# Kernel tuning notes

Hardware: AMD Instinct MI355X
Metric: run time of the kernel (lower is better)

Reference implementation:

```python
import jax, jax.numpy as jnp
import numpy as np

IN_DIM = 256
OUT_DIM = 64   # per-head dim
NUM_HEADS = 8
B = 8
N = 1024


def setup_inputs() -> dict:
    key = jax.random.key(0)
    k_adj, k_h, kq, kk, kv, kbq, kbk, kbv = jax.random.split(key, 8)
    adj_matrix = jax.random.randint(k_adj, (N, N), 0, 2, dtype=jnp.int32)
    h = jax.random.normal(k_h, (B, N, IN_DIM), dtype=jnp.float32)
    s = 1.0 / np.sqrt(IN_DIM)
    Wq = jax.random.normal(kq, (IN_DIM, OUT_DIM * NUM_HEADS), dtype=jnp.float32) * s
    Wk = jax.random.normal(kk, (IN_DIM, OUT_DIM * NUM_HEADS), dtype=jnp.float32) * s
    Wv = jax.random.normal(kv, (IN_DIM, OUT_DIM * NUM_HEADS), dtype=jnp.float32) * s
    bq = jax.random.normal(kbq, (OUT_DIM * NUM_HEADS,), dtype=jnp.float32) * 0.01
    bk = jax.random.normal(kbk, (OUT_DIM * NUM_HEADS,), dtype=jnp.float32) * 0.01
    bv = jax.random.normal(kbv, (OUT_DIM * NUM_HEADS,), dtype=jnp.float32) * 0.01
    return {"adj_matrix": adj_matrix, "h": h, "Wq": Wq, "bq": bq,
            "Wk": Wk, "bk": bk, "Wv": Wv, "bv": bv}


def reference(adj_matrix, h, Wq, bq, Wk, bk, Wv, bv):
    B_, N_, _ = h.shape
    H, D = NUM_HEADS, OUT_DIM
    Qh = (h @ Wq + bq).reshape(B_, N_, H, D)
    Kh = (h @ Wk + bk).reshape(B_, N_, H, D)
    Vh = (h @ Wv + bv).reshape(B_, N_, H, D)
    scores = jnp.einsum('bnhd,bmhd->bhnm', Qh, Kh) / jnp.sqrt(jnp.float32(D))
    # adjacency mask broadcast over batch and heads (neigh_attention=True)
    scores = jnp.where(adj_matrix[None, None, :, :] == 0, -jnp.inf, scores)
    attn = jax.nn.softmax(scores, axis=-1)
    out = jnp.einsum('bhnm,bmhd->bnhd', attn, Vh)
    return out.reshape(B_, N_, H * D)
```

## Files before the change

### kernel.cpp

```cpp
#include <hip/hip_runtime.h>
#include <hip/hip_bf16.h>
#include <math.h>

#define IN_DIM 256
#define HD     512
#define NHEADS 8
#define DH     64
#define NSEQ   1024
#define BATCH  8

#define QSCALE 0.18033688011112042f

typedef unsigned short u16;
typedef unsigned int   u32;
typedef short bf16x8 __attribute__((ext_vector_type(8)));
typedef float f32x4  __attribute__((ext_vector_type(4)));
typedef float f32x16 __attribute__((ext_vector_type(16)));
typedef unsigned int u32x2 __attribute__((ext_vector_type(2)));

#if __has_builtin(__builtin_amdgcn_exp2f)
#define EXP2(x) __builtin_amdgcn_exp2f(x)
#else
#define EXP2(x) __expf(0.69314718056f * (x))
#endif

static __device__ __forceinline__ u16 f2bf(float x) {
    u32 u = __builtin_bit_cast(u32, x);
    u += 0x7FFFu + ((u >> 16) & 1u);
    return (u16)(u >> 16);
}
static __device__ __forceinline__ u32 pk(u16 a, u16 b) {
    return (u32)a | ((u32)b << 16);
}
static __device__ __forceinline__ u32 cvtpk(float a, float b) {
    __hip_bfloat162 t = __float22bfloat162_rn(make_float2(a, b));
    u32 r; __builtin_memcpy(&r, &t, 4);
    return r;
}
static __device__ __forceinline__ f32x16 maskinit(uint4 a, uint4 b) {
    f32x16 c;
    u32 ws[8] = {a.x, a.y, a.z, a.w, b.x, b.y, b.z, b.w};
#pragma unroll
    for (int i = 0; i < 8; ++i) {
        c[2 * i]     = __builtin_bit_cast(float, ws[i] << 16);
        c[2 * i + 1] = __builtin_bit_cast(float, ws[i] & 0xFFFF0000u);
    }
    return c;
}

static __device__ __forceinline__ void pswap(u32 &a, u32 &b) {
#if __has_builtin(__builtin_amdgcn_permlane32_swap)
    u32x2 r = __builtin_amdgcn_permlane32_swap(a, b, false, false);
    a = r.x; b = r.y;
#else
    const bool hi = (threadIdx.x & 32) != 0;
    u32 as = (u32)__shfl_xor((int)a, 32, 64);
    u32 bs = (u32)__shfl_xor((int)b, 32, 64);
    u32 na = hi ? bs : a;
    u32 nb = hi ? b  : as;
    a = na; b = nb;
#endif
}

#define MFMA32(a, b, c) __builtin_amdgcn_mfma_f32_32x32x16_bf16(a, b, c, 0, 0, 0)

static __device__ __forceinline__ float sm_pack(const f32x16 s0, const f32x16 s1,
                                                bf16x8* pb) {
    float p0[16], p1[16];
#pragma unroll
    for (int r = 0; r < 16; ++r) p0[r] = EXP2(s0[r]);
#pragma unroll
    for (int r = 0; r < 16; ++r) p1[r] = EXP2(s1[r]);
    float t0 = (((p0[0] + p0[1]) + (p0[2] + p0[3])) + ((p0[4] + p0[5]) + (p0[6] + p0[7])))
             + (((p0[8] + p0[9]) + (p0[10] + p0[11])) + ((p0[12] + p0[13]) + (p0[14] + p0[15])));
    float t1 = (((p1[0] + p1[1]) + (p1[2] + p1[3])) + ((p1[4] + p1[5]) + (p1[6] + p1[7])))
             + (((p1[8] + p1[9]) + (p1[10] + p1[11])) + ((p1[12] + p1[13]) + (p1[14] + p1[15])));
    uint4 w0, w1, w2, w3;
    w0.x = cvtpk(p0[0], p0[1]);   w0.y = cvtpk(p0[2], p0[3]);
    w0.z = cvtpk(p0[4], p0[5]);   w0.w = cvtpk(p0[6], p0[7]);
    w1.x = cvtpk(p0[8], p0[9]);   w1.y = cvtpk(p0[10], p0[11]);
    w1.z = cvtpk(p0[12], p0[13]); w1.w = cvtpk(p0[14], p0[15]);
    w2.x = cvtpk(p1[0], p1[1]);   w2.y = cvtpk(p1[2], p1[3]);
    w2.z = cvtpk(p1[4], p1[5]);   w2.w = cvtpk(p1[6], p1[7]);
    w3.x = cvtpk(p1[8], p1[9]);   w3.y = cvtpk(p1[10], p1[11]);
    w3.z = cvtpk(p1[12], p1[13]); w3.w = cvtpk(p1[14], p1[15]);
    pswap(w0.x, w1.x); pswap(w0.y, w1.y); pswap(w0.z, w1.z); pswap(w0.w, w1.w);
    pswap(w2.x, w3.x); pswap(w2.y, w3.y); pswap(w2.z, w3.z); pswap(w2.w, w3.w);
    pb[0] = __builtin_bit_cast(bf16x8, w0);
    pb[1] = __builtin_bit_cast(bf16x8, w1);
    pb[2] = __builtin_bit_cast(bf16x8, w2);
    pb[3] = __builtin_bit_cast(bf16x8, w3);
    return t0 + t1;
}

__global__ __launch_bounds__(256)
void wtrans_kernel(const float* __restrict__ Wq, const float* __restrict__ Wk,
                   const float* __restrict__ Wv, u16* __restrict__ Wt)
{
    __shared__ float tile[64 * 65];
    const int bid = blockIdx.x, tid = threadIdx.x;
    const int k0 = (bid & 3) * 64, n0 = ((bid >> 2) & 7) * 64, wsel = bid >> 5;
    const float* W = (wsel == 0) ? Wq : (wsel == 1) ? Wk : Wv;
    u16* Out = Wt + (size_t)wsel * HD * IN_DIM;

    const int r = tid >> 2, c0 = (tid & 3) * 16;
#pragma unroll
    for (int j = 0; j < 16; j += 4) {
        float4 v = *(const float4*)(W + (size_t)(k0 + r) * HD + n0 + c0 + j);
        tile[r * 65 + c0 + j + 0] = v.x; tile[r * 65 + c0 + j + 1] = v.y;
        tile[r * 65 + c0 + j + 2] = v.z; tile[r * 65 + c0 + j + 3] = v.w;
    }
    __syncthreads();
    const int n = tid >> 2, ks = (tid & 3) * 16;
    u16 o[16];
#pragma unroll
    for (int j = 0; j < 16; ++j) o[j] = f2bf(tile[(ks + j) * 65 + n]);
    uint4 u0, u1;
    u0.x = pk(o[0], o[1]);   u0.y = pk(o[2], o[3]);
    u0.z = pk(o[4], o[5]);   u0.w = pk(o[6], o[7]);
    u1.x = pk(o[8], o[9]);   u1.y = pk(o[10], o[11]);
    u1.z = pk(o[12], o[13]); u1.w = pk(o[14], o[15]);
    u16* dst = Out + (size_t)(n0 + n) * IN_DIM + k0 + ks;
    *(uint4*)(dst) = u0;
    *(uint4*)(dst + 8) = u1;
}

__global__ __launch_bounds__(256, 4)
void gemm_mask_kernel(const float* __restrict__ h, const u16* __restrict__ Wt,
                      const int* __restrict__ adj,
                      const float* __restrict__ bq, const float* __restrict__ bk,
                      const float* __restrict__ bv,
                      u16* __restrict__ Qg, u16* __restrict__ Kg,
                      u16* __restrict__ Vtg, u16* __restrict__ Madd2)
{
    __shared__ u16 pool[64 * 64 + 3 * 64 * 64];
    const int tid = threadIdx.x;

    if (blockIdx.y >= 8) {
        int* tile = (int*)pool;
        const int abid = (blockIdx.y - 8) * 128 + blockIdx.x;
        const int tR = abid >> 4, tC = abid & 15;
        const int r = tid >> 2, cg = (tid & 3) * 16;
        const int* src = adj + (size_t)(tR * 64 + r) * NSEQ + tC * 64 + cg;
#pragma unroll
        for (int j = 0; j < 16; j += 4) {
            int4 a = *(const int4*)(src + j);
            tile[r * 65 + cg + j + 0] = a.x; tile[r * 65 + cg + j + 1] = a.y;
            tile[r * 65 + cg + j + 2] = a.z; tile[r * 65 + cg + j + 3] = a.w;
        }
        __syncthreads();
        const int q = tid >> 2, p0 = (tid & 3) * 16;
        u16 o[16];
#pragma unroll
        for (int j = 0; j < 16; ++j) {
            const int p = p0 + j;
            const int c = 32 * (p >> 5) + (p & 3) + 4 * ((p >> 4) & 1) + 8 * ((p >> 2) & 3);
            o[j] = (tile[q * 65 + c] == 0) ? (u16)0xFF7F : (u16)0;
        }
        uint4 u0, u1;
        u0.x = pk(o[0], o[1]);   u0.y = pk(o[2], o[3]);
        u0.z = pk(o[4], o[5]);   u0.w = pk(o[6], o[7]);
        u1.x = pk(o[8], o[9]);   u1.y = pk(o[10], o[11]);
        u1.z = pk(o[12], o[13]); u1.w = pk(o[14], o[15]);
        u16* dst = Madd2 + (size_t)(tR * 64 + q) * NSEQ + tC * 64 + p0;
        *(uint4*)(dst) = u0;
        *(uint4*)(dst + 8) = u1;
        return;
    }

    u16* As = pool;
    u16* Bs = pool + 64 * 64;

    const int m0 = blockIdx.x * 64;
    const int hh = blockIdx.y;
    const int n0 = hh * 64;

    const int w = tid >> 6, lane = tid & 63;
    const int l31 = lane & 31, half = lane >> 5;
    const int mh = w & 1, nh = w >> 1;
    const int s7 = l31 & 7;

    f32x16 acc[3] = {};

    const int arw = tid >> 2, acg = (tid & 3) * 2;
    const int brw = tid & 63, bgrp = tid >> 6;
    const float* srcA = h + (size_t)(m0 + arw) * IN_DIM;

    for (int kk = 0; kk < IN_DIM; kk += 64) {
        __syncthreads();
#pragma unroll
        for (int g = 0; g < 2; ++g) {
            const float* p = srcA + kk + (acg + g) * 8;
            float4 v0 = *(const float4*)(p);
            float4 v1 = *(const float4*)(p + 4);
            uint4 u;
            u.x = cvtpk(v0.x, v0.y); u.y = cvtpk(v0.z, v0.w);
            u.z = cvtpk(v1.x, v1.y); u.w = cvtpk(v1.z, v1.w);
            *(uint4*)&As[arw * 64 + (((acg + g) ^ (arw & 7)) * 8)] = u;
        }
#pragma unroll
        for (int i = 0; i < 6; ++i) {
            const int gc = bgrp * 6 + i;
            const int wh = gc >> 3, c8 = gc & 7;
            *(uint4*)&Bs[wh * 4096 + brw * 64 + ((c8 ^ (brw & 7)) * 8)] =
                *(const uint4*)(Wt + (size_t)wh * HD * IN_DIM +
                                (size_t)(n0 + brw) * IN_DIM + kk + c8 * 8);
        }
        __syncthreads();
        const int arow = (32 * mh + l31) * 64;
        const int brow = (32 * nh + l31) * 64;
#pragma unroll
        for (int s = 0; s < 4; ++s) {
            const int g = ((s * 2 + half) ^ s7) * 8;
            bf16x8 a = *(const bf16x8*)&As[arow + g];
#pragma unroll
            for (int wh = 0; wh < 3; ++wh) {
                bf16x8 b = *(const bf16x8*)&Bs[wh * 4096 + brow + g];
                acc[wh] = __builtin_amdgcn_mfma_f32_32x32x16_bf16(a, b, acc[wh], 0, 0, 0);
            }
        }
    }

    for (int which = 0; which < 2; ++which) {
        u16* T = pool;
        const float* bias = (which == 0) ? bq : bk;
        u16* Out = (which == 0) ? Qg : Kg;
        const float scale = (which == 0) ? QSCALE : 1.0f;
        const float bvv = bias[n0 + 32 * nh + l31];
        __syncthreads();
#pragma unroll
        for (int r = 0; r < 16; ++r) {
            const int row = 32 * mh + 4 * half + (r & 3) + 8 * (r >> 2);
            T[row * 72 + 32 * nh + l31] = f2bf((acc[which][r] + bvv) * scale);
        }
        __syncthreads();
        const int row = tid >> 2, qc = (tid & 3) * 16;
        u16* dst = Out + (size_t)(m0 + row) * HD + n0 + qc;
        const u16* srcT = &T[row * 72 + qc];
        *(uint4*)(dst)     = *(const uint4*)(srcT);
        *(uint4*)(dst + 8) = *(const uint4*)(srcT + 8);
    }

    {
        u16* T = pool;
        const int d = 32 * nh + l31;
        const float bvv = bv[n0 + d];
        __syncthreads();
#pragma unroll
        for (int g = 0; g < 4; ++g) {
            ushort4 o;
            o.x = f2bf(acc[2][4 * g + 0] + bvv);
            o.y = f2bf(acc[2][4 * g + 1] + bvv);
            o.z = f2bf(acc[2][4 * g + 2] + bvv);
            o.w = f2bf(acc[2][4 * g + 3] + bvv);
            *(ushort4*)&T[d * 72 + 32 * mh + 16 * half + 4 * g] = o;
        }
        __syncthreads();
        const int b = m0 >> 10, nloc = m0 & 1023;
        const int dd = tid >> 2, c = (tid & 3) * 16;
        u16* dst = Vtg + ((size_t)(b * NHEADS + hh) * DH + dd) * NSEQ + nloc + c;
        *(uint4*)(dst)     = *(uint4*)&T[dd * 72 + c];
        *(uint4*)(dst + 8) = *(uint4*)&T[dd * 72 + c + 8];
    }
}

__global__ __launch_bounds__(256, 1)
void attn_kernel(const u16* __restrict__ Madd2, const u16* __restrict__ Qg,
                 const u16* __restrict__ Kg, const u16* __restrict__ Vtg,
                 float* __restrict__ out)
{
    __shared__ u16 Ks[2][64 * 64];
    __shared__ u16 Vs[2][64 * 64];

    const int tid = threadIdx.x;
    const int w = tid >> 6, lane = tid & 63;
    const int l31 = lane & 31, half = lane >> 5;
    const int bh = blockIdx.x, qt = blockIdx.y;
    const int b = bh >> 3;
    const int n0 = qt * 256;
    const size_t rowbase = (size_t)b * NSEQ;
    const int colbase = (bh & 7) * DH;
    const int q7 = l31 & 7;
    const int qA = w * 64 + l31;
    const int qB = qA + 32;

    const u16* qga = Qg + (rowbase + n0 + qA) * HD + colbase;
    const u16* qgb = Qg + (rowbase + n0 + qB) * HD + colbase;
    bf16x8 qbA[4], qbB[4];
#pragma unroll
    for (int s = 0; s < 4; ++s) {
        qbA[s] = *(const bf16x8*)(qga + s * 16 + half * 8);
        qbB[s] = *(const bf16x8*)(qgb + s * 16 + half * 8);
    }

    const int srow = tid >> 2, cp = (tid & 3) * 2;
    const int swc0 = ((cp ^ (srow & 7)) * 8), swc1 = (((cp + 1) ^ (srow & 7)) * 8);
    const u16* kgp = Kg + (rowbase + srow) * HD + colbase + cp * 8;
    const u16* vgp = Vtg + ((size_t)bh * DH + srow) * NSEQ + cp * 8;
    const u16* mrowA = Madd2 + (size_t)(n0 + qA) * NSEQ + half * 16;
    const u16* mrowB = Madd2 + (size_t)(n0 + qB) * NSEQ + half * 16;

    uint4 mA0a = *(const uint4*)(mrowA);
    uint4 mA0b = *(const uint4*)(mrowA + 8);
    uint4 mA1a = *(const uint4*)(mrowA + 32);
    uint4 mA1b = *(const uint4*)(mrowA + 40);
    uint4 mB0a = *(const uint4*)(mrowB);
    uint4 mB0b = *(const uint4*)(mrowB + 8);
    uint4 mB1a = *(const uint4*)(mrowB + 32);
    uint4 mB1b = *(const uint4*)(mrowB + 40);

    uint4 s0k0, s0k1, s0v0, s0v1;
    uint4 s1k0, s1k1, s1v0, s1v1;
    s0k0 = *(const uint4*)kgp;       s0k1 = *(const uint4*)(kgp + 8);
    s0v0 = *(const uint4*)vgp;       s0v1 = *(const uint4*)(vgp + 8);
    *(uint4*)&Ks[0][srow * 64 + swc0] = s0k0;
    *(uint4*)&Ks[0][srow * 64 + swc1] = s0k1;
    *(uint4*)&Vs[0][srow * 64 + swc0] = s0v0;
    *(uint4*)&Vs[0][srow * 64 + swc1] = s0v1;
    s1k0 = *(const uint4*)(kgp + (size_t)64 * HD);
    s1k1 = *(const uint4*)(kgp + (size_t)64 * HD + 8);
    s1v0 = *(const uint4*)(vgp + 64);
    s1v1 = *(const uint4*)(vgp + 64 + 8);
    __syncthreads();

    float lA = 0.f, lB = 0.f;
    f32x16 OA0 = {}, OA1 = {}, OB0 = {}, OB1 = {};

#define CHUNK(CH, CUR, KW, KL)                                                 \
    {                                                                          \
        f32x16 sA0 = maskinit(mA0a, mA0b);                                     \
        f32x16 sA1 = maskinit(mA1a, mA1b);                                     \
        f32x16 sB0 = maskinit(mB0a, mB0b);                                     \
        f32x16 sB1 = maskinit(mB1a, mB1b);                                     \
        if ((CH) < 15) {                                                       \
            const u16* ma = mrowA + ((CH) + 1) * 64;                           \
            const u16* mb = mrowB + ((CH) + 1) * 64;                           \
            mA0a = *(const uint4*)(ma);      mA0b = *(const uint4*)(ma + 8);   \
            mA1a = *(const uint4*)(ma + 32); mA1b = *(const uint4*)(ma + 40);  \
            mB0a = *(const uint4*)(mb);      mB0b = *(const uint4*)(mb + 8);   \
            mB1a = *(const uint4*)(mb + 32); mB1b = *(const uint4*)(mb + 40);  \
        }                                                                      \
        _Pragma("unroll")                                                      \
        for (int s = 0; s < 4; ++s) {                                          \
            const int g = ((s * 2 + half) ^ q7) * 8;                           \
            bf16x8 ka0 = *(const bf16x8*)&Ks[CUR][l31 * 64 + g];               \
            bf16x8 ka1 = *(const bf16x8*)&Ks[CUR][(32 + l31) * 64 + g];        \
            sA0 = MFMA32(ka0, qbA[s], sA0);                                    \
            sA1 = MFMA32(ka1, qbA[s], sA1);                                    \
            sB0 = MFMA32(ka0, qbB[s], sB0);                                    \
            sB1 = MFMA32(ka1, qbB[s], sB1);                                    \
        }                                                                      \
        if ((CH) < 15) {                                                       \
            *(uint4*)&Ks[1 - (CUR)][srow * 64 + swc0] = KW##k0;                \
            *(uint4*)&Ks[1 - (CUR)][srow * 64 + swc1] = KW##k1;                \
            *(uint4*)&Vs[1 - (CUR)][srow * 64 + swc0] = KW##v0;                \
            *(uint4*)&Vs[1 - (CUR)][srow * 64 + swc1] = KW##v1;                \
        }                                                                      \
        if ((CH) < 14) {                                                       \
            const size_t ko = (size_t)((CH) + 2) * 64 * HD;                    \
            const int    vo = ((CH) + 2) * 64;                                 \
            KL##k0 = *(const uint4*)(kgp + ko);                                \
            KL##k1 = *(const uint4*)(kgp + ko + 8);                            \
            KL##v0 = *(const uint4*)(vgp + vo);                                \
            KL##v1 = *(const uint4*)(vgp + vo + 8);                            \
        }                                                                      \
        bf16x8 pbA[4], pbB[4];                                                 \
        lA += sm_pack(sA0, sA1, pbA);                                          \
        lB += sm_pack(sB0, sB1, pbB);                                          \
        _Pragma("unroll")                                                      \
        for (int s = 0; s < 4; ++s) {                                          \
            const int g = ((s * 2 + half) ^ q7) * 8;                           \
            bf16x8 va0 = *(const bf16x8*)&Vs[CUR][l31 * 64 + g];               \
            bf16x8 va1 = *(const bf16x8*)&Vs[CUR][(32 + l31) * 64 + g];        \
            OA0 = MFMA32(va0, pbA[s], OA0);                                    \
            OA1 = MFMA32(va1, pbA[s], OA1);                                    \
            OB0 = MFMA32(va0, pbB[s], OB0);                                    \
            OB1 = MFMA32(va1, pbB[s], OB1);                                    \
        }                                                                      \
        __syncthreads();                                                       \
    }

    for (int ch = 0; ch < 16; ch += 2) {
        CHUNK(ch,     0, s1, s0)
        CHUNK(ch + 1, 1, s0, s1)
    }
#undef CHUNK

    lA += __shfl_xor(lA, 32, 64);
    lB += __shfl_xor(lB, 32, 64);
    const float invA = 1.0f / lA;
    const float invB = 1.0f / lB;

    float* orowA = out + (rowbase + n0 + qA) * HD + colbase;
    float* orowB = out + (rowbase + n0 + qB) * HD + colbase;
#pragma unroll
    for (int g = 0; g < 4; ++g) {
        const int d0 = 4 * half + 8 * g;
        float4 a0, a1, b0, b1;
        a0.x = OA0[4 * g + 0] * invA; a0.y = OA0[4 * g + 1] * invA;
        a0.z = OA0[4 * g + 2] * invA; a0.w = OA0[4 * g + 3] * invA;
        a1.x = OA1[4 * g + 0] * invA; a1.y = OA1[4 * g + 1] * invA;
        a1.z = OA1[4 * g + 2] * invA; a1.w = OA1[4 * g + 3] * invA;
        b0.x = OB0[4 * g + 0] * invB; b0.y = OB0[4 * g + 1] * invB;
        b0.z = OB0[4 * g + 2] * invB; b0.w = OB0[4 * g + 3] * invB;
        b1.x = OB1[4 * g + 0] * invB; b1.y = OB1[4 * g + 1] * invB;
        b1.z = OB1[4 * g + 2] * invB; b1.w = OB1[4 * g + 3] * invB;
        *(float4*)(orowA + d0)      = a0;
        *(float4*)(orowA + 32 + d0) = a1;
        *(float4*)(orowB + d0)      = b0;
        *(float4*)(orowB + 32 + d0) = b1;
    }
}

extern "C" void kernel_launch(void* const* d_in, const int* in_sizes, int n_in,
                              void* d_out, int out_size, void* d_ws, size_t ws_size,
                              hipStream_t stream) {
    const int*   adj = (const int*)d_in[0];
    const float* h   = (const float*)d_in[1];
    const float* Wq  = (const float*)d_in[2];
    const float* bq  = (const float*)d_in[3];
    const float* Wk  = (const float*)d_in[4];
    const float* bk  = (const float*)d_in[5];
    const float* Wv  = (const float*)d_in[6];
    const float* bv  = (const float*)d_in[7];
    float* outp = (float*)d_out;

    u16* Wt    = (u16*)d_ws;
    u16* Qg    = Wt + (size_t)3 * HD * IN_DIM;
    u16* Kg    = Qg + (size_t)BATCH * NSEQ * HD;
    u16* Vtg   = Kg + (size_t)BATCH * NSEQ * HD;
    u16* Madd2 = Vtg + (size_t)BATCH * NSEQ * HD;
    (void)ws_size;

    wtrans_kernel<<<96, 256, 0, stream>>>(Wq, Wk, Wv, Wt);
    gemm_mask_kernel<<<dim3(BATCH * NSEQ / 64, 10), 256, 0, stream>>>(
        h, Wt, adj, bq, bk, bv, Qg, Kg, Vtg, Madd2);
    attn_kernel<<<dim3(BATCH * NHEADS, NSEQ / 256), 256, 0, stream>>>(
        Madd2, Qg, Kg, Vtg, outp);
}
```

Measured before the change: 136.0 us.

## Split attention key range across two wave teams with LDS reduction

The attention block grows to 512 threads in two teams of four waves. Each team processes half of the key/value sequence with its own double-buffered LDS tiles. Partial outputs and row sums are then reduced through LDS before team 0 normalizes and writes. This doubles the waves per block to improve latency hiding and shortens the serial chunk loop, at the cost of extra LDS, a cross-team reduction, and possible register pressure under the new launch bounds. The scheme relies on the softmax having no running-max rescale, so the two halves' partial sums can simply be added.

```diff
diff --git a/kernel.cpp b/kernel.cpp
--- a/kernel.cpp
+++ b/kernel.cpp
@@ -264,16 +264,17 @@
     }
 }
 
-__global__ __launch_bounds__(256, 1)
+__global__ __launch_bounds__(512, 2)
 void attn_kernel(const u16* __restrict__ Madd2, const u16* __restrict__ Qg,
                  const u16* __restrict__ Kg, const u16* __restrict__ Vtg,
                  float* __restrict__ out)
 {
-    __shared__ u16 Ks[2][64 * 64];
-    __shared__ u16 Vs[2][64 * 64];
+    __shared__ __align__(16) u16 Ks[2][2][64 * 64];
+    __shared__ __align__(16) u16 Vs[2][2][64 * 64];
 
     const int tid = threadIdx.x;
     const int w = tid >> 6, lane = tid & 63;
+    const int team = w >> 2, wq = w & 3;
     const int l31 = lane & 31, half = lane >> 5;
     const int bh = blockIdx.x, qt = blockIdx.y;
     const int b = bh >> 3;
@@ -281,8 +282,9 @@
     const size_t rowbase = (size_t)b * NSEQ;
     const int colbase = (bh & 7) * DH;
     const int q7 = l31 & 7;
-    const int qA = w * 64 + l31;
+    const int qA = wq * 64 + l31;
     const int qB = qA + 32;
+    const int cbase = team * 8;
 
     const u16* qga = Qg + (rowbase + n0 + qA) * HD + colbase;
     const u16* qgb = Qg + (rowbase + n0 + qB) * HD + colbase;
@@ -293,12 +295,14 @@
         qbB[s] = *(const bf16x8*)(qgb + s * 16 + half * 8);
     }
 
-    const int srow = tid >> 2, cp = (tid & 3) * 2;
+    const int ttid = tid & 255;
+    const int srow = ttid >> 2, cp = (ttid & 3) * 2;
     const int swc0 = ((cp ^ (srow & 7)) * 8), swc1 = (((cp + 1) ^ (srow & 7)) * 8);
-    const u16* kgp = Kg + (rowbase + srow) * HD + colbase + cp * 8;
-    const u16* vgp = Vtg + ((size_t)bh * DH + srow) * NSEQ + cp * 8;
-    const u16* mrowA = Madd2 + (size_t)(n0 + qA) * NSEQ + half * 16;
-    const u16* mrowB = Madd2 + (size_t)(n0 + qB) * NSEQ + half * 16;
+    const u16* kgp = Kg + (rowbase + srow) * HD + colbase + cp * 8 +
+                     (size_t)cbase * 64 * HD;
+    const u16* vgp = Vtg + ((size_t)bh * DH + srow) * NSEQ + cp * 8 + cbase * 64;
+    const u16* mrowA = Madd2 + (size_t)(n0 + qA) * NSEQ + half * 16 + cbase * 64;
+    const u16* mrowB = Madd2 + (size_t)(n0 + qB) * NSEQ + half * 16 + cbase * 64;
 
     uint4 mA0a = *(const uint4*)(mrowA);
     uint4 mA0b = *(const uint4*)(mrowA + 8);
@@ -313,10 +317,10 @@
     uint4 s1k0, s1k1, s1v0, s1v1;
     s0k0 = *(const uint4*)kgp;       s0k1 = *(const uint4*)(kgp + 8);
     s0v0 = *(const uint4*)vgp;       s0v1 = *(const uint4*)(vgp + 8);
-    *(uint4*)&Ks[0][srow * 64 + swc0] = s0k0;
-    *(uint4*)&Ks[0][srow * 64 + swc1] = s0k1;
-    *(uint4*)&Vs[0][srow * 64 + swc0] = s0v0;
-    *(uint4*)&Vs[0][srow * 64 + swc1] = s0v1;
+    *(uint4*)&Ks[team][0][srow * 64 + swc0] = s0k0;
+    *(uint4*)&Ks[team][0][srow * 64 + swc1] = s0k1;
+    *(uint4*)&Vs[team][0][srow * 64 + swc0] = s0v0;
+    *(uint4*)&Vs[team][0][srow * 64 + swc1] = s0v1;
     s1k0 = *(const uint4*)(kgp + (size_t)64 * HD);
     s1k1 = *(const uint4*)(kgp + (size_t)64 * HD + 8);
     s1v0 = *(const uint4*)(vgp + 64);
@@ -332,7 +336,7 @@
         f32x16 sA1 = maskinit(mA1a, mA1b);                                     \
         f32x16 sB0 = maskinit(mB0a, mB0b);                                     \
         f32x16 sB1 = maskinit(mB1a, mB1b);                                     \
-        if ((CH) < 15) {                                                       \
+        if ((CH) < 7) {                                                        \
             const u16* ma = mrowA + ((CH) + 1) * 64;                           \
             const u16* mb = mrowB + ((CH) + 1) * 64;                           \
             mA0a = *(const uint4*)(ma);      mA0b = *(const uint4*)(ma + 8);   \
@@ -343,20 +347,20 @@
         _Pragma("unroll")                                                      \
         for (int s = 0; s < 4; ++s) {                                          \
             const int g = ((s * 2 + half) ^ q7) * 8;                           \
-            bf16x8 ka0 = *(const bf16x8*)&Ks[CUR][l31 * 64 + g];               \
-            bf16x8 ka1 = *(const bf16x8*)&Ks[CUR][(32 + l31) * 64 + g];        \
+            bf16x8 ka0 = *(const bf16x8*)&Ks[team][CUR][l31 * 64 + g];         \
+            bf16x8 ka1 = *(const bf16x8*)&Ks[team][CUR][(32 + l31) * 64 + g];  \
             sA0 = MFMA32(ka0, qbA[s], sA0);                                    \
             sA1 = MFMA32(ka1, qbA[s], sA1);                                    \
             sB0 = MFMA32(ka0, qbB[s], sB0);                                    \
             sB1 = MFMA32(ka1, qbB[s], sB1);                                    \
         }                                                                      \
-        if ((CH) < 15) {                                                       \
-            *(uint4*)&Ks[1 - (CUR)][srow * 64 + swc0] = KW##k0;                \
-            *(uint4*)&Ks[1 - (CUR)][srow * 64 + swc1] = KW##k1;                \
-            *(uint4*)&Vs[1 - (CUR)][srow * 64 + swc0] = KW##v0;                \
-            *(uint4*)&Vs[1 - (CUR)][srow * 64 + swc1] = KW##v1;                \
+        if ((CH) < 7) {                                                        \
+            *(uint4*)&Ks[team][1 - (CUR)][srow * 64 + swc0] = KW##k0;          \
+            *(uint4*)&Ks[team][1 - (CUR)][srow * 64 + swc1] = KW##k1;          \
+            *(uint4*)&Vs[team][1 - (CUR)][srow * 64 + swc0] = KW##v0;          \
+            *(uint4*)&Vs[team][1 - (CUR)][srow * 64 + swc1] = KW##v1;          \
         }                                                                      \
-        if ((CH) < 14) {                                                       \
+        if ((CH) < 6) {                                                        \
             const size_t ko = (size_t)((CH) + 2) * 64 * HD;                    \
             const int    vo = ((CH) + 2) * 64;                                 \
             KL##k0 = *(const uint4*)(kgp + ko);                                \
@@ -370,8 +374,8 @@
         _Pragma("unroll")                                                      \
         for (int s = 0; s < 4; ++s) {                                          \
             const int g = ((s * 2 + half) ^ q7) * 8;                           \
-            bf16x8 va0 = *(const bf16x8*)&Vs[CUR][l31 * 64 + g];               \
-            bf16x8 va1 = *(const bf16x8*)&Vs[CUR][(32 + l31) * 64 + g];        \
+            bf16x8 va0 = *(const bf16x8*)&Vs[team][CUR][l31 * 64 + g];         \
+            bf16x8 va1 = *(const bf16x8*)&Vs[team][CUR][(32 + l31) * 64 + g];  \
             OA0 = MFMA32(va0, pbA[s], OA0);                                    \
             OA1 = MFMA32(va1, pbA[s], OA1);                                    \
             OB0 = MFMA32(va0, pbB[s], OB0);                                    \
@@ -380,35 +384,92 @@
         __syncthreads();                                                       \
     }
 
-    for (int ch = 0; ch < 16; ch += 2) {
+    for (int ch = 0; ch < 8; ch += 2) {
         CHUNK(ch,     0, s1, s0)
         CHUNK(ch + 1, 1, s0, s1)
     }
 #undef CHUNK
 
-    lA += __shfl_xor(lA, 32, 64);
-    lB += __shfl_xor(lB, 32, 64);
-    const float invA = 1.0f / lA;
-    const float invB = 1.0f / lB;
-
-    float* orowA = out + (rowbase + n0 + qA) * HD + colbase;
-    float* orowB = out + (rowbase + n0 + qB) * HD + colbase;
-#pragma unroll
-    for (int g = 0; g < 4; ++g) {
-        const int d0 = 4 * half + 8 * g;
-        float4 a0, a1, b0, b1;
-        a0.x = OA0[4 * g + 0] * invA; a0.y = OA0[4 * g + 1] * invA;
-        a0.z = OA0[4 * g + 2] * invA; a0.w = OA0[4 * g + 3] * invA;
-        a1.x = OA1[4 * g + 0] * invA; a1.y = OA1[4 * g + 1] * invA;
-        a1.z = OA1[4 * g + 2] * invA; a1.w = OA1[4 * g + 3] * invA;
-        b0.x = OB0[4 * g + 0] * invB; b0.y = OB0[4 * g + 1] * invB;
-        b0.z = OB0[4 * g + 2] * invB; b0.w = OB0[4 * g + 3] * invB;
-        b1.x = OB1[4 * g + 0] * invB; b1.y = OB1[4 * g + 1] * invB;
-        b1.z = OB1[4 * g + 2] * invB; b1.w = OB1[4 * g + 3] * invB;
-        *(float4*)(orowA + d0)      = a0;
-        *(float4*)(orowA + 32 + d0) = a1;
-        *(float4*)(orowB + d0)      = b0;
-        *(float4*)(orowB + 32 + d0) = b1;
+    float4* Oex = (float4*)&Ks[0][0][0];
+    float*  Lex = (float*)&Vs[0][0][0];
+
+    if (team == 1) {
+#pragma unroll
+        for (int g = 0; g < 4; ++g) {
+            float4 t0, t1;
+            t0.x = OA0[4 * g + 0]; t0.y = OA0[4 * g + 1];
+            t0.z = OA0[4 * g + 2]; t0.w = OA0[4 * g + 3];
+            t1.x = OA1[4 * g + 0]; t1.y = OA1[4 * g + 1];
+            t1.z = OA1[4 * g + 2]; t1.w = OA1[4 * g + 3];
+            Oex[(wq * 8 + g) * 64 + lane]     = t0;
+            Oex[(wq * 8 + 4 + g) * 64 + lane] = t1;
+        }
+        Lex[wq * 128 + lane]      = lA;
+        Lex[wq * 128 + 64 + lane] = lB;
+    }
+    __syncthreads();
+    if (team == 0) {
+        lA += Lex[wq * 128 + lane];
+        lB += Lex[wq * 128 + 64 + lane];
+#pragma unroll
+        for (int g = 0; g < 4; ++g) {
+            float4 t0 = Oex[(wq * 8 + g) * 64 + lane];
+            float4 t1 = Oex[(wq * 8 + 4 + g) * 64 + lane];
+            OA0[4 * g + 0] += t0.x; OA0[4 * g + 1] += t0.y;
+            OA0[4 * g + 2] += t0.z; OA0[4 * g + 3] += t0.w;
+            OA1[4 * g + 0] += t1.x; OA1[4 * g + 1] += t1.y;
+            OA1[4 * g + 2] += t1.z; OA1[4 * g + 3] += t1.w;
+        }
+    }
+    __syncthreads();
+    if (team == 1) {
+#pragma unroll
+        for (int g = 0; g < 4; ++g) {
+            float4 t0, t1;
+            t0.x = OB0[4 * g + 0]; t0.y = OB0[4 * g + 1];
+            t0.z = OB0[4 * g + 2]; t0.w = OB0[4 * g + 3];
+            t1.x = OB1[4 * g + 0]; t1.y = OB1[4 * g + 1];
+            t1.z = OB1[4 * g + 2]; t1.w = OB1[4 * g + 3];
+            Oex[(wq * 8 + g) * 64 + lane]     = t0;
+            Oex[(wq * 8 + 4 + g) * 64 + lane] = t1;
+        }
+    }
+    __syncthreads();
+    if (team == 0) {
+#pragma unroll
+        for (int g = 0; g < 4; ++g) {
+            float4 t0 = Oex[(wq * 8 + g) * 64 + lane];
+            float4 t1 = Oex[(wq * 8 + 4 + g) * 64 + lane];
+            OB0[4 * g + 0] += t0.x; OB0[4 * g + 1] += t0.y;
+            OB0[4 * g + 2] += t0.z; OB0[4 * g + 3] += t0.w;
+            OB1[4 * g + 0] += t1.x; OB1[4 * g + 1] += t1.y;
+            OB1[4 * g + 2] += t1.z; OB1[4 * g + 3] += t1.w;
+        }
+
+        lA += __shfl_xor(lA, 32, 64);
+        lB += __shfl_xor(lB, 32, 64);
+        const float invA = 1.0f / lA;
+        const float invB = 1.0f / lB;
+
+        float* orowA = out + (rowbase + n0 + qA) * HD + colbase;
+        float* orowB = out + (rowbase + n0 + qB) * HD + colbase;
+#pragma unroll
+        for (int g = 0; g < 4; ++g) {
+            const int d0 = 4 * half + 8 * g;
+            float4 a0, a1, b0, b1;
+            a0.x = OA0[4 * g + 0] * invA; a0.y = OA0[4 * g + 1] * invA;
+            a0.z = OA0[4 * g + 2] * invA; a0.w = OA0[4 * g + 3] * invA;
+            a1.x = OA1[4 * g + 0] * invA; a1.y = OA1[4 * g + 1] * invA;
+            a1.z = OA1[4 * g + 2] * invA; a1.w = OA1[4 * g + 3] * invA;
+            b0.x = OB0[4 * g + 0] * invB; b0.y = OB0[4 * g + 1] * invB;
+            b0.z = OB0[4 * g + 2] * invB; b0.w = OB0[4 * g + 3] * invB;
+            b1.x = OB1[4 * g + 0] * invB; b1.y = OB1[4 * g + 1] * invB;
+            b1.z = OB1[4 * g + 2] * invB; b1.w = OB1[4 * g + 3] * invB;
+            *(float4*)(orowA + d0)      = a0;
+            *(float4*)(orowA + 32 + d0) = a1;
+            *(float4*)(orowB + d0)      = b0;
+            *(float4*)(orowB + 32 + d0) = b1;
+        }
     }
 }
 
@@ -435,6 +496,6 @@
     wtrans_kernel<<<96, 256, 0, stream>>>(Wq, Wk, Wv, Wt);
     gemm_mask_kernel<<<dim3(BATCH * NSEQ / 64, 10), 256, 0, stream>>>(
         h, Wt, adj, bq, bk, bv, Qg, Kg, Vtg, Madd2);
-    attn_kernel<<<dim3(BATCH * NHEADS, NSEQ / 256), 256, 0, stream>>>(
+    attn_kernel<<<dim3(BATCH * NHEADS, NSEQ / 256), 512, 0, stream>>>(
         Madd2, Qg, Kg, Vtg, outp);
 }
```

Result: slower. 184.9 us (+36.0%).

## Split attention keys across two wave teams, drop LDS staging, reduce partials

Applied to the files above, without the earlier changes.

The attention kernel now handles 128 queries per block instead of 256, and splits the key range between two teams of two waves each (split-K). K and V fragments are loaded straight from global memory into registers, where before they were double-buffered through LDS with a barrier per chunk. Partial outputs and row sums are combined through shared memory at the end. This doubles the grid, allows two blocks per CU and removes per-chunk synchronisation, at the cost of uncoalesced or duplicated global K/V reads that now depend on the cache, plus a final reduction step.

```diff
diff --git a/kernel.cpp b/kernel.cpp
--- a/kernel.cpp
+++ b/kernel.cpp
@@ -64,33 +64,21 @@
 
 #define MFMA32(a, b, c) __builtin_amdgcn_mfma_f32_32x32x16_bf16(a, b, c, 0, 0, 0)
 
-static __device__ __forceinline__ float sm_pack(const f32x16 s0, const f32x16 s1,
-                                                bf16x8* pb) {
-    float p0[16], p1[16];
-#pragma unroll
-    for (int r = 0; r < 16; ++r) p0[r] = EXP2(s0[r]);
-#pragma unroll
-    for (int r = 0; r < 16; ++r) p1[r] = EXP2(s1[r]);
-    float t0 = (((p0[0] + p0[1]) + (p0[2] + p0[3])) + ((p0[4] + p0[5]) + (p0[6] + p0[7])))
-             + (((p0[8] + p0[9]) + (p0[10] + p0[11])) + ((p0[12] + p0[13]) + (p0[14] + p0[15])));
-    float t1 = (((p1[0] + p1[1]) + (p1[2] + p1[3])) + ((p1[4] + p1[5]) + (p1[6] + p1[7])))
-             + (((p1[8] + p1[9]) + (p1[10] + p1[11])) + ((p1[12] + p1[13]) + (p1[14] + p1[15])));
-    uint4 w0, w1, w2, w3;
-    w0.x = cvtpk(p0[0], p0[1]);   w0.y = cvtpk(p0[2], p0[3]);
-    w0.z = cvtpk(p0[4], p0[5]);   w0.w = cvtpk(p0[6], p0[7]);
-    w1.x = cvtpk(p0[8], p0[9]);   w1.y = cvtpk(p0[10], p0[11]);
-    w1.z = cvtpk(p0[12], p0[13]); w1.w = cvtpk(p0[14], p0[15]);
-    w2.x = cvtpk(p1[0], p1[1]);   w2.y = cvtpk(p1[2], p1[3]);
-    w2.z = cvtpk(p1[4], p1[5]);   w2.w = cvtpk(p1[6], p1[7]);
-    w3.x = cvtpk(p1[8], p1[9]);   w3.y = cvtpk(p1[10], p1[11]);
-    w3.z = cvtpk(p1[12], p1[13]); w3.w = cvtpk(p1[14], p1[15]);
+static __device__ __forceinline__ float sm_pack_half(const f32x16 st, bf16x8* pb) {
+    float p[16];
+#pragma unroll
+    for (int r = 0; r < 16; ++r) p[r] = EXP2(st[r]);
+    float t = (((p[0] + p[1]) + (p[2] + p[3])) + ((p[4] + p[5]) + (p[6] + p[7])))
+            + (((p[8] + p[9]) + (p[10] + p[11])) + ((p[12] + p[13]) + (p[14] + p[15])));
+    uint4 w0, w1;
+    w0.x = cvtpk(p[0], p[1]);   w0.y = cvtpk(p[2], p[3]);
+    w0.z = cvtpk(p[4], p[5]);   w0.w = cvtpk(p[6], p[7]);
+    w1.x = cvtpk(p[8], p[9]);   w1.y = cvtpk(p[10], p[11]);
+    w1.z = cvtpk(p[12], p[13]); w1.w = cvtpk(p[14], p[15]);
     pswap(w0.x, w1.x); pswap(w0.y, w1.y); pswap(w0.z, w1.z); pswap(w0.w, w1.w);
-    pswap(w2.x, w3.x); pswap(w2.y, w3.y); pswap(w2.z, w3.z); pswap(w2.w, w3.w);
     pb[0] = __builtin_bit_cast(bf16x8, w0);
     pb[1] = __builtin_bit_cast(bf16x8, w1);
-    pb[2] = __builtin_bit_cast(bf16x8, w2);
-    pb[3] = __builtin_bit_cast(bf16x8, w3);
-    return t0 + t1;
+    return t;
 }
 
 __global__ __launch_bounds__(256)
@@ -264,25 +252,26 @@
     }
 }
 
-__global__ __launch_bounds__(256, 1)
+__global__ __launch_bounds__(256, 2)
 void attn_kernel(const u16* __restrict__ Madd2, const u16* __restrict__ Qg,
                  const u16* __restrict__ Kg, const u16* __restrict__ Vtg,
                  float* __restrict__ out)
 {
-    __shared__ u16 Ks[2][64 * 64];
-    __shared__ u16 Vs[2][64 * 64];
+    __shared__ __align__(16) float4 Oex[2048 + 1984];
+    __shared__ float Lex[256];
 
     const int tid = threadIdx.x;
     const int w = tid >> 6, lane = tid & 63;
+    const int team = w >> 1, wq = w & 1;
     const int l31 = lane & 31, half = lane >> 5;
     const int bh = blockIdx.x, qt = blockIdx.y;
     const int b = bh >> 3;
-    const int n0 = qt * 256;
+    const int n0 = qt * 128;
     const size_t rowbase = (size_t)b * NSEQ;
     const int colbase = (bh & 7) * DH;
-    const int q7 = l31 & 7;
-    const int qA = w * 64 + l31;
+    const int qA = wq * 64 + l31;
     const int qB = qA + 32;
+    const int cbase = team * 8;
 
     const u16* qga = Qg + (rowbase + n0 + qA) * HD + colbase;
     const u16* qgb = Qg + (rowbase + n0 + qB) * HD + colbase;
@@ -293,12 +282,12 @@
         qbB[s] = *(const bf16x8*)(qgb + s * 16 + half * 8);
     }
 
-    const int srow = tid >> 2, cp = (tid & 3) * 2;
-    const int swc0 = ((cp ^ (srow & 7)) * 8), swc1 = (((cp + 1) ^ (srow & 7)) * 8);
-    const u16* kgp = Kg + (rowbase + srow) * HD + colbase + cp * 8;
-    const u16* vgp = Vtg + ((size_t)bh * DH + srow) * NSEQ + cp * 8;
-    const u16* mrowA = Madd2 + (size_t)(n0 + qA) * NSEQ + half * 16;
-    const u16* mrowB = Madd2 + (size_t)(n0 + qB) * NSEQ + half * 16;
+    const u16* kb0 = Kg + (rowbase + cbase * 64 + l31) * HD + colbase + half * 8;
+    const u16* kb1 = kb0 + 32 * HD;
+    const u16* vb0 = Vtg + ((size_t)bh * DH + l31) * NSEQ + cbase * 64 + half * 8;
+    const u16* vb1 = vb0 + 32 * NSEQ;
+    const u16* mrowA = Madd2 + (size_t)(n0 + qA) * NSEQ + cbase * 64 + half * 16;
+    const u16* mrowB = Madd2 + (size_t)(n0 + qB) * NSEQ + cbase * 64 + half * 16;
 
     uint4 mA0a = *(const uint4*)(mrowA);
     uint4 mA0b = *(const uint4*)(mrowA + 8);
@@ -309,106 +298,143 @@
     uint4 mB1a = *(const uint4*)(mrowB + 32);
     uint4 mB1b = *(const uint4*)(mrowB + 40);
 
-    uint4 s0k0, s0k1, s0v0, s0v1;
-    uint4 s1k0, s1k1, s1v0, s1v1;
-    s0k0 = *(const uint4*)kgp;       s0k1 = *(const uint4*)(kgp + 8);
-    s0v0 = *(const uint4*)vgp;       s0v1 = *(const uint4*)(vgp + 8);
-    *(uint4*)&Ks[0][srow * 64 + swc0] = s0k0;
-    *(uint4*)&Ks[0][srow * 64 + swc1] = s0k1;
-    *(uint4*)&Vs[0][srow * 64 + swc0] = s0v0;
-    *(uint4*)&Vs[0][srow * 64 + swc1] = s0v1;
-    s1k0 = *(const uint4*)(kgp + (size_t)64 * HD);
-    s1k1 = *(const uint4*)(kgp + (size_t)64 * HD + 8);
-    s1v0 = *(const uint4*)(vgp + 64);
-    s1v1 = *(const uint4*)(vgp + 64 + 8);
-    __syncthreads();
-
     float lA = 0.f, lB = 0.f;
     f32x16 OA0 = {}, OA1 = {}, OB0 = {}, OB1 = {};
 
-#define CHUNK(CH, CUR, KW, KL)                                                 \
-    {                                                                          \
-        f32x16 sA0 = maskinit(mA0a, mA0b);                                     \
-        f32x16 sA1 = maskinit(mA1a, mA1b);                                     \
-        f32x16 sB0 = maskinit(mB0a, mB0b);                                     \
-        f32x16 sB1 = maskinit(mB1a, mB1b);                                     \
-        if ((CH) < 15) {                                                       \
-            const u16* ma = mrowA + ((CH) + 1) * 64;                           \
-            const u16* mb = mrowB + ((CH) + 1) * 64;                           \
-            mA0a = *(const uint4*)(ma);      mA0b = *(const uint4*)(ma + 8);   \
-            mA1a = *(const uint4*)(ma + 32); mA1b = *(const uint4*)(ma + 40);  \
-            mB0a = *(const uint4*)(mb);      mB0b = *(const uint4*)(mb + 8);   \
-            mB1a = *(const uint4*)(mb + 32); mB1b = *(const uint4*)(mb + 40);  \
-        }                                                                      \
-        _Pragma("unroll")                                                      \
-        for (int s = 0; s < 4; ++s) {                                          \
-            const int g = ((s * 2 + half) ^ q7) * 8;                           \
-            bf16x8 ka0 = *(const bf16x8*)&Ks[CUR][l31 * 64 + g];               \
-            bf16x8 ka1 = *(const bf16x8*)&Ks[CUR][(32 + l31) * 64 + g];        \
-            sA0 = MFMA32(ka0, qbA[s], sA0);                                    \
-            sA1 = MFMA32(ka1, qbA[s], sA1);                                    \
-            sB0 = MFMA32(ka0, qbB[s], sB0);                                    \
-            sB1 = MFMA32(ka1, qbB[s], sB1);                                    \
-        }                                                                      \
-        if ((CH) < 15) {                                                       \
-            *(uint4*)&Ks[1 - (CUR)][srow * 64 + swc0] = KW##k0;                \
-            *(uint4*)&Ks[1 - (CUR)][srow * 64 + swc1] = KW##k1;                \
-            *(uint4*)&Vs[1 - (CUR)][srow * 64 + swc0] = KW##v0;                \
-            *(uint4*)&Vs[1 - (CUR)][srow * 64 + swc1] = KW##v1;                \
-        }                                                                      \
-        if ((CH) < 14) {                                                       \
-            const size_t ko = (size_t)((CH) + 2) * 64 * HD;                    \
-            const int    vo = ((CH) + 2) * 64;                                 \
-            KL##k0 = *(const uint4*)(kgp + ko);                                \
-            KL##k1 = *(const uint4*)(kgp + ko + 8);                            \
-            KL##v0 = *(const uint4*)(vgp + vo);                                \
-            KL##v1 = *(const uint4*)(vgp + vo + 8);                            \
-        }                                                                      \
-        bf16x8 pbA[4], pbB[4];                                                 \
-        lA += sm_pack(sA0, sA1, pbA);                                          \
-        lB += sm_pack(sB0, sB1, pbB);                                          \
-        _Pragma("unroll")                                                      \
-        for (int s = 0; s < 4; ++s) {                                          \
-            const int g = ((s * 2 + half) ^ q7) * 8;                           \
-            bf16x8 va0 = *(const bf16x8*)&Vs[CUR][l31 * 64 + g];               \
-            bf16x8 va1 = *(const bf16x8*)&Vs[CUR][(32 + l31) * 64 + g];        \
-            OA0 = MFMA32(va0, pbA[s], OA0);                                    \
-            OA1 = MFMA32(va1, pbA[s], OA1);                                    \
-            OB0 = MFMA32(va0, pbB[s], OB0);                                    \
-            OB1 = MFMA32(va1, pbB[s], OB1);                                    \
-        }                                                                      \
-        __syncthreads();                                                       \
-    }
-
-    for (int ch = 0; ch < 16; ch += 2) {
-        CHUNK(ch,     0, s1, s0)
-        CHUNK(ch + 1, 1, s0, s1)
-    }
-#undef CHUNK
-
-    lA += __shfl_xor(lA, 32, 64);
-    lB += __shfl_xor(lB, 32, 64);
-    const float invA = 1.0f / lA;
-    const float invB = 1.0f / lB;
-
-    float* orowA = out + (rowbase + n0 + qA) * HD + colbase;
-    float* orowB = out + (rowbase + n0 + qB) * HD + colbase;
-#pragma unroll
-    for (int g = 0; g < 4; ++g) {
-        const int d0 = 4 * half + 8 * g;
-        float4 a0, a1, b0, b1;
-        a0.x = OA0[4 * g + 0] * invA; a0.y = OA0[4 * g + 1] * invA;
-        a0.z = OA0[4 * g + 2] * invA; a0.w = OA0[4 * g + 3] * invA;
-        a1.x = OA1[4 * g + 0] * invA; a1.y = OA1[4 * g + 1] * invA;
-        a1.z = OA1[4 * g + 2] * invA; a1.w = OA1[4 * g + 3] * invA;
-        b0.x = OB0[4 * g + 0] * invB; b0.y = OB0[4 * g + 1] * invB;
-        b0.z = OB0[4 * g + 2] * invB; b0.w = OB0[4 * g + 3] * invB;
-        b1.x = OB1[4 * g + 0] * invB; b1.y = OB1[4 * g + 1] * invB;
-        b1.z = OB1[4 * g + 2] * invB; b1.w = OB1[4 * g + 3] * invB;
-        *(float4*)(orowA + d0)      = a0;
-        *(float4*)(orowA + 32 + d0) = a1;
-        *(float4*)(orowB + d0)      = b0;
-        *(float4*)(orowB + 32 + d0) = b1;
+    for (int ch = 0; ch < 8; ++ch) {
+        const u16* kr0 = kb0 + (size_t)ch * 64 * HD;
+        const u16* kr1 = kb1 + (size_t)ch * 64 * HD;
+        const u16* vr0 = vb0 + ch * 64;
+        const u16* vr1 = vb1 + ch * 64;
+
+        f32x16 sA0 = maskinit(mA0a, mA0b);
+        f32x16 sB0 = maskinit(mB0a, mB0b);
+        {
+            bf16x8 k0 = *(const bf16x8*)(kr0);
+            bf16x8 k1 = *(const bf16x8*)(kr0 + 16);
+            bf16x8 k2 = *(const bf16x8*)(kr0 + 32);
+            bf16x8 k3 = *(const bf16x8*)(kr0 + 48);
+            sA0 = MFMA32(k0, qbA[0], sA0); sB0 = MFMA32(k0, qbB[0], sB0);
+            sA0 = MFMA32(k1, qbA[1], sA0); sB0 = MFMA32(k1, qbB[1], sB0);
+            sA0 = MFMA32(k2, qbA[2], sA0); sB0 = MFMA32(k2, qbB[2], sB0);
+            sA0 = MFMA32(k3, qbA[3], sA0); sB0 = MFMA32(k3, qbB[3], sB0);
+        }
+        bf16x8 pbA[2], pbB[2];
+        lA += sm_pack_half(sA0, pbA);
+        lB += sm_pack_half(sB0, pbB);
+
+        f32x16 sA1 = maskinit(mA1a, mA1b);
+        f32x16 sB1 = maskinit(mB1a, mB1b);
+        if (ch < 7) {
+            const u16* ma = mrowA + (ch + 1) * 64;
+            const u16* mb = mrowB + (ch + 1) * 64;
+            mA0a = *(const uint4*)(ma);      mA0b = *(const uint4*)(ma + 8);
+            mA1a = *(const uint4*)(ma + 32); mA1b = *(const uint4*)(ma + 40);
+            mB0a = *(const uint4*)(mb);      mB0b = *(const uint4*)(mb + 8);
+            mB1a = *(const uint4*)(mb + 32); mB1b = *(const uint4*)(mb + 40);
+        }
+        {
+            bf16x8 k0 = *(const bf16x8*)(kr1);
+            bf16x8 k1 = *(const bf16x8*)(kr1 + 16);
+            bf16x8 k2 = *(const bf16x8*)(kr1 + 32);
+            bf16x8 k3 = *(const bf16x8*)(kr1 + 48);
+            sA1 = MFMA32(k0, qbA[0], sA1); sB1 = MFMA32(k0, qbB[0], sB1);
+            sA1 = MFMA32(k1, qbA[1], sA1); sB1 = MFMA32(k1, qbB[1], sB1);
+            sA1 = MFMA32(k2, qbA[2], sA1); sB1 = MFMA32(k2, qbB[2], sB1);
+            sA1 = MFMA32(k3, qbA[3], sA1); sB1 = MFMA32(k3, qbB[3], sB1);
+        }
+
+        {
+            bf16x8 v00 = *(const bf16x8*)(vr0);
+            bf16x8 v10 = *(const bf16x8*)(vr1);
+            bf16x8 v01 = *(const bf16x8*)(vr0 + 16);
+            bf16x8 v11 = *(const bf16x8*)(vr1 + 16);
+            OA0 = MFMA32(v00, pbA[0], OA0); OA1 = MFMA32(v10, pbA[0], OA1);
+            OB0 = MFMA32(v00, pbB[0], OB0); OB1 = MFMA32(v10, pbB[0], OB1);
+            OA0 = MFMA32(v01, pbA[1], OA0); OA1 = MFMA32(v11, pbA[1], OA1);
+            OB0 = MFMA32(v01, pbB[1], OB0); OB1 = MFMA32(v11, pbB[1], OB1);
+        }
+
+        lA += sm_pack_half(sA1, pbA);
+        lB += sm_pack_half(sB1, pbB);
+        {
+            bf16x8 v00 = *(const bf16x8*)(vr0 + 32);
+            bf16x8 v10 = *(const bf16x8*)(vr1 + 32);
+            bf16x8 v01 = *(const bf16x8*)(vr0 + 48);
+            bf16x8 v11 = *(const bf16x8*)(vr1 + 48);
+            OA0 = MFMA32(v00, pbA[0], OA0); OA1 = MFMA32(v10, pbA[0], OA1);
+            OB0 = MFMA32(v00, pbB[0], OB0); OB1 = MFMA32(v10, pbB[0], OB1);
+            OA0 = MFMA32(v01, pbA[1], OA0); OA1 = MFMA32(v11, pbA[1], OA1);
+            OB0 = MFMA32(v01, pbB[1], OB0); OB1 = MFMA32(v11, pbB[1], OB1);
+        }
+    }
+
+    if (team == 1) {
+        const int base = wq * 16;
+#pragma unroll
+        for (int g = 0; g < 4; ++g) {
+            float4 t;
+            t.x = OA0[4 * g + 0]; t.y = OA0[4 * g + 1];
+            t.z = OA0[4 * g + 2]; t.w = OA0[4 * g + 3];
+            Oex[(base + g) * 64 + lane] = t;
+            t.x = OA1[4 * g + 0]; t.y = OA1[4 * g + 1];
+            t.z = OA1[4 * g + 2]; t.w = OA1[4 * g + 3];
+            Oex[(base + 4 + g) * 64 + lane] = t;
+            t.x = OB0[4 * g + 0]; t.y = OB0[4 * g + 1];
+            t.z = OB0[4 * g + 2]; t.w = OB0[4 * g + 3];
+            Oex[(base + 8 + g) * 64 + lane] = t;
+            t.x = OB1[4 * g + 0]; t.y = OB1[4 * g + 1];
+            t.z = OB1[4 * g + 2]; t.w = OB1[4 * g + 3];
+            Oex[(base + 12 + g) * 64 + lane] = t;
+        }
+        Lex[(wq * 2 + 0) * 64 + lane] = lA;
+        Lex[(wq * 2 + 1) * 64 + lane] = lB;
+    }
+    __syncthreads();
+    if (team == 0) {
+        const int base = wq * 16;
+        lA += Lex[(wq * 2 + 0) * 64 + lane];
+        lB += Lex[(wq * 2 + 1) * 64 + lane];
+#pragma unroll
+        for (int g = 0; g < 4; ++g) {
+            float4 t0 = Oex[(base + g) * 64 + lane];
+            float4 t1 = Oex[(base + 4 + g) * 64 + lane];
+            float4 t2 = Oex[(base + 8 + g) * 64 + lane];
+            float4 t3 = Oex[(base + 12 + g) * 64 + lane];
+            OA0[4 * g + 0] += t0.x; OA0[4 * g + 1] += t0.y;
+            OA0[4 * g + 2] += t0.z; OA0[4 * g + 3] += t0.w;
+            OA1[4 * g + 0] += t1.x; OA1[4 * g + 1] += t1.y;
+            OA1[4 * g + 2] += t1.z; OA1[4 * g + 3] += t1.w;
+            OB0[4 * g + 0] += t2.x; OB0[4 * g + 1] += t2.y;
+            OB0[4 * g + 2] += t2.z; OB0[4 * g + 3] += t2.w;
+            OB1[4 * g + 0] += t3.x; OB1[4 * g + 1] += t3.y;
+            OB1[4 * g + 2] += t3.z; OB1[4 * g + 3] += t3.w;
+        }
+
+        lA += __shfl_xor(lA, 32, 64);
+        lB += __shfl_xor(lB, 32, 64);
+        const float invA = 1.0f / lA;
+        const float invB = 1.0f / lB;
+
+        float* orowA = out + (rowbase + n0 + qA) * HD + colbase;
+        float* orowB = out + (rowbase + n0 + qB) * HD + colbase;
+#pragma unroll
+        for (int g = 0; g < 4; ++g) {
+            const int d0 = 4 * half + 8 * g;
+            float4 a0, a1, b0, b1;
+            a0.x = OA0[4 * g + 0] * invA; a0.y = OA0[4 * g + 1] * invA;
+            a0.z = OA0[4 * g + 2] * invA; a0.w = OA0[4 * g + 3] * invA;
+            a1.x = OA1[4 * g + 0] * invA; a1.y = OA1[4 * g + 1] * invA;
+            a1.z = OA1[4 * g + 2] * invA; a1.w = OA1[4 * g + 3] * invA;
+            b0.x = OB0[4 * g + 0] * invB; b0.y = OB0[4 * g + 1] * invB;
+            b0.z = OB0[4 * g + 2] * invB; b0.w = OB0[4 * g + 3] * invB;
+            b1.x = OB1[4 * g + 0] * invB; b1.y = OB1[4 * g + 1] * invB;
+            b1.z = OB1[4 * g + 2] * invB; b1.w = OB1[4 * g + 3] * invB;
+            *(float4*)(orowA + d0)      = a0;
+            *(float4*)(orowA + 32 + d0) = a1;
+            *(float4*)(orowB + d0)      = b0;
+            *(float4*)(orowB + 32 + d0) = b1;
+        }
     }
 }
 
@@ -435,6 +461,6 @@
     wtrans_kernel<<<96, 256, 0, stream>>>(Wq, Wk, Wv, Wt);
     gemm_mask_kernel<<<dim3(BATCH * NSEQ / 64, 10), 256, 0, stream>>>(
         h, Wt, adj, bq, bk, bv, Qg, Kg, Vtg, Madd2);
-    attn_kernel<<<dim3(BATCH * NHEADS, NSEQ / 256), 256, 0, stream>>>(
+    attn_kernel<<<dim3(BATCH * NHEADS, NSEQ / 128), 256, 0, stream>>>(
         Madd2, Qg, Kg, Vtg, outp);
 }
```

Result: slower. 151.0 us (+11.1%).
